# Performance work log

Hardware: AMD Instinct MI355X
Metric: run time of the kernel (lower is better)

The kernel has to match this reference:

```python
import jax, jax.numpy as jnp
import numpy as np

B, N, D, H = 8, 1024, 768, 12
HD = D // H  # head_dim = 64


def setup_inputs() -> dict:
    key = jax.random.key(0)
    k1, k2 = jax.random.split(key)
    x = jax.random.normal(k1, (B, N, D), dtype=jnp.float32)
    W_qkv = jax.random.normal(k2, (D, 3 * D), dtype=jnp.float32) * 0.02
    b_qkv = jnp.zeros((3 * D,), dtype=jnp.float32)
    return {"x": x, "W_qkv": W_qkv, "b_qkv": b_qkv}


def reference(x, W_qkv, b_qkv):
    b, n, d = x.shape
    qkv = x @ W_qkv + b_qkv                      # [B, N, 3D]
    qkv = qkv.reshape(b, n, 3, H, HD)
    qkv = jnp.transpose(qkv, (2, 0, 3, 1, 4))    # [3, B, H, N, HD]
    q, k, v = qkv[0], qkv[1], qkv[2]
    scale = 1.0 / jnp.sqrt(jnp.float32(HD))
    scores = jnp.einsum('bhqd,bhkd->bhqk', q, k) * scale   # [B, H, N, N]
    attn = jax.nn.softmax(scores, axis=-1)
    out = jnp.einsum('bhqk,bhkd->bhqd', attn, v)            # [B, H, N, HD]
    # concat heads along last dim (same as torch.cat over head outputs)
    return jnp.transpose(out, (0, 2, 1, 3)).reshape(b, n, d)
```

## Files before the change

### kernel.cpp

```cpp
#include <hip/hip_runtime.h>
#include <stdint.h>

#define BB 8
#define NN 1024
#define DDIM 768
#define HH 12
#define HDIM 64
#define D3 2304
#define MM 8192

typedef __attribute__((ext_vector_type(4))) float f32x4;
typedef __attribute__((ext_vector_type(16))) float f32x16;
typedef __attribute__((ext_vector_type(8))) __bf16 bf16x8;
typedef __attribute__((ext_vector_type(8))) unsigned short u16x8;
typedef __attribute__((ext_vector_type(4))) unsigned short u16x4;

__device__ __forceinline__ unsigned short f2bf(float f) {
  unsigned int u = __float_as_uint(f);
  u += 0x7FFFu + ((u >> 16) & 1u);
  return (unsigned short)(u >> 16);
}

__device__ __forceinline__ void gload_lds16(const void* g, void* l) {
  __builtin_amdgcn_global_load_lds((const __attribute__((address_space(1))) void*)g,
                                   (__attribute__((address_space(3))) void*)l,
                                   16, 0, 0);
}

__device__ __forceinline__ unsigned cvtpk_bf16(float lo, float hi) {
  unsigned r;
  asm("v_cvt_pk_bf16_f32 %0, %1, %2" : "=v"(r) : "v"(lo), "v"(hi));
  return r;
}

__device__ __forceinline__ bf16x8 mkfrag(unsigned a, unsigned b, unsigned c, unsigned d) {
  union { unsigned u[4]; bf16x8 v; } x;
  x.u[0] = a; x.u[1] = b; x.u[2] = c; x.u[3] = d;
  return x.v;
}

#if __has_builtin(__builtin_amdgcn_exp2f)
#define EXP2(x) __builtin_amdgcn_exp2f(x)
#else
#define EXP2(x) exp2f(x)
#endif

#define QSCL 0.18033688f

__global__ void k_prep(const float4* __restrict__ x, u16x4* __restrict__ xb,
                       const float* __restrict__ W, unsigned short* __restrict__ Wt) {
  __shared__ float tile[32][33];
  const int bid = blockIdx.x;
  if (bid < 6144) {
    int i = bid * 256 + threadIdx.x;
    float4 v = x[i];
    u16x4 o;
    o[0] = f2bf(v.x); o[1] = f2bf(v.y); o[2] = f2bf(v.z); o[3] = f2bf(v.w);
    xb[i] = o;
    return;
  }
  const int bid2 = bid - 6144;
  const int tx = threadIdx.x & 31, ty = threadIdx.x >> 5;
  const int n0 = (bid2 % 72) * 32;
  const int k0 = (bid2 / 72) * 32;
  for (int i = 0; i < 4; ++i) {
    int k = k0 + ty + i * 8;
    tile[ty + i * 8][tx] = W[(size_t)k * D3 + n0 + tx];
  }
  __syncthreads();
  for (int i = 0; i < 4; ++i) {
    int n = n0 + ty + i * 8;
    Wt[(size_t)n * DDIM + k0 + tx] = f2bf(tile[tx][ty + i * 8]);
  }
}

__global__ __launch_bounds__(256, 3)
void k_gemm(const unsigned short* __restrict__ A, const unsigned short* __restrict__ Bt,
            const float* __restrict__ bias, unsigned short* __restrict__ C) {
  __shared__ char lds[48 * 1024];
  const int t = threadIdx.x, lane = t & 63, wid = t >> 6;
  const int orig = blockIdx.x;
  const int xcd = orig & 7, tt = orig >> 3;
  const int m0 = (xcd * 8 + (tt & 7)) * 128;
  const int n0 = (tt >> 3) * 128;
  const int wr = wid >> 1, wc = wid & 1;
  const int grp = lane >> 4, lc = lane & 15;

  f32x4 acc[4][4];
  for (int i = 0; i < 4; ++i)
    for (int j = 0; j < 4; ++j) acc[i][j] = (f32x4)(0.0f);

  auto STAGE = [&](int buf, int kt) {
    char* Ab = lds + buf * 16384;
    char* Bb = Ab + 8192;
#pragma unroll
    for (int i = 0; i < 2; ++i) {
      int chunk = wid * 2 + i;
      int g = chunk * 64 + lane;
      int row = g >> 2, c16 = (g & 3) << 4;
      gload_lds16((const char*)A + (size_t)(m0 + row) * 1536 + kt * 64 + c16, Ab + chunk * 1024);
      gload_lds16((const char*)Bt + (size_t)(n0 + row) * 1536 + kt * 64 + c16, Bb + chunk * 1024);
    }
  };

  STAGE(0, 0);
  asm volatile("s_waitcnt vmcnt(0)" ::: "memory");
  __builtin_amdgcn_s_barrier();

  int cur = 0;
  for (int kt = 0; kt < 24; ++kt) {
    const int nxt = (cur == 2) ? 0 : cur + 1;
    if (kt < 23) {
      STAGE(nxt, kt + 1);
      asm volatile("s_waitcnt vmcnt(4)" ::: "memory");
    } else {
      asm volatile("s_waitcnt vmcnt(0)" ::: "memory");
    }
    __builtin_amdgcn_s_barrier();

    const char* As = lds + cur * 16384;
    const char* Bs = As + 8192;
    bf16x8 af[4], bfr[4];
#pragma unroll
    for (int f = 0; f < 4; ++f) {
      af[f]  = *(const bf16x8*)(As + (wr * 64 + f * 16 + lc) * 64 + grp * 16);
      bfr[f] = *(const bf16x8*)(Bs + (wc * 64 + f * 16 + lc) * 64 + grp * 16);
    }
    __builtin_amdgcn_s_setprio(1);
#pragma unroll
    for (int mf = 0; mf < 4; ++mf)
#pragma unroll
      for (int nf = 0; nf < 4; ++nf)
        acc[mf][nf] = __builtin_amdgcn_mfma_f32_16x16x32_bf16(af[mf], bfr[nf], acc[mf][nf], 0, 0, 0);
    __builtin_amdgcn_s_setprio(0);
    cur = nxt;
  }

  float bv[4];
  float qs[4];
  for (int nf = 0; nf < 4; ++nf) {
    bv[nf] = bias[n0 + wc * 64 + nf * 16 + lc];
    qs[nf] = (n0 + wc * 64 + nf * 16) < DDIM ? QSCL : 1.0f;
  }
  for (int mf = 0; mf < 4; ++mf)
    for (int nf = 0; nf < 4; ++nf)
      for (int i = 0; i < 4; ++i) {
        int r = m0 + wr * 64 + mf * 16 + grp * 4 + i;
        int c = n0 + wc * 64 + nf * 16 + lc;
        C[(size_t)r * D3 + c] = f2bf((acc[mf][nf][i] + bv[nf]) * qs[nf]);
      }
}

__global__ void k_pack(const unsigned short* __restrict__ qkv,
                       unsigned short* __restrict__ kp, unsigned short* __restrict__ vp) {
  __shared__ unsigned short KT[64][68];
  __shared__ unsigned short VT[64][68];
  const int bh = blockIdx.x, kt = blockIdx.y;
  const int b = bh / HH, h = bh % HH;
  const int n0 = kt * 64;
  const int t = threadIdx.x;
#pragma unroll
  for (int it = 0; it < 2; ++it) {
    int id = it * 256 + t;
    int row = id >> 3, seg = id & 7;
    const unsigned short* src = qkv + (size_t)(b * NN + n0 + row) * D3 + DDIM + h * HDIM + seg * 8;
    *(u16x8*)&KT[row][seg * 8] = *(const u16x8*)src;
    *(u16x8*)&VT[row][seg * 8] = *(const u16x8*)(src + DDIM);
  }
  __syncthreads();
  const size_t base = (size_t)(bh * 16 + kt) * 4096;
#pragma unroll
  for (int it = 0; it < 2; ++it) {
    int w = it * 256 + t;
    int c = w >> 6, lane = w & 63;
    int hi2 = lane >> 5, l31 = lane & 31;
    int half = c & 1, quad = c >> 1;
    {
      int row = half * 32 + l31, seg = quad * 2 + hi2;
      *(u16x8*)(kp + base + (size_t)w * 8) = *(const u16x8*)&KT[row][seg * 8];
    }
    {
      int d = half * 32 + l31, nloc = quad * 16 + hi2 * 8;
      u16x8 o;
#pragma unroll
      for (int j = 0; j < 8; ++j) o[j] = VT[nloc + j][d];
      *(u16x8*)(vp + base + (size_t)w * 8) = o;
    }
  }
}

__global__ __launch_bounds__(256, 3)
void k_attn(const unsigned short* __restrict__ qkv,
            const unsigned short* __restrict__ kp, const unsigned short* __restrict__ vp,
            float* __restrict__ out) {
  __shared__ char lds[48 * 1024];
  const int lane = threadIdx.x & 63, wid = threadIdx.x >> 6;
  const int orig = blockIdx.x;
  const int wg = (orig & 7) * 96 + (orig >> 3);
  const int bh = wg >> 3, qt = wg & 7;
  const int b = bh / HH, h = bh % HH;
  const int q0 = qt * 128 + wid * 32;
  const int l31 = lane & 31, hi = lane >> 5;

  auto STAGE = [&](int bi, int kt2) {
    char* buf = lds + bi * 16384;
    const char* gk = (const char*)kp + (size_t)(bh * 16 + kt2) * 8192 + lane * 16;
    const char* gv = (const char*)vp + (size_t)(bh * 16 + kt2) * 8192 + lane * 16;
#pragma unroll
    for (int i = 0; i < 4; ++i) {
      int e = wid * 4 + i;
      const char* g = (e < 8) ? (gk + e * 1024) : (gv + (e - 8) * 1024);
      char* l = (e < 8) ? (buf + e * 1024) : (buf + 8192 + (e - 8) * 1024);
      gload_lds16(g, l);
    }
  };

  STAGE(0, 0);

  bf16x8 qf[4];
  const char* qbase = (const char*)qkv + ((size_t)(b * NN + q0 + l31) * D3 + h * HDIM) * 2;
#pragma unroll
  for (int ds_ = 0; ds_ < 4; ++ds_)
    qf[ds_] = *(const bf16x8*)(qbase + ds_ * 32 + hi * 16);

  f32x16 acc0 = (f32x16)(0.0f), acc1 = (f32x16)(0.0f);
  float l = 0.0f;

  asm volatile("s_waitcnt vmcnt(0)" ::: "memory");
  __builtin_amdgcn_s_barrier();

  int cur = 0;
  for (int kt = 0; kt < 16; ++kt) {
    const int nxt = (cur == 2) ? 0 : cur + 1;
    if (kt < 15) {
      STAGE(nxt, kt + 1);
      asm volatile("s_waitcnt vmcnt(4)" ::: "memory");
    } else {
      asm volatile("s_waitcnt vmcnt(0)" ::: "memory");
    }
    __builtin_amdgcn_s_barrier();

    const char* Kc = lds + cur * 16384;
    const char* Vc = Kc + 8192;

    bf16x8 kf[4][2];
#pragma unroll
    for (int ds_ = 0; ds_ < 4; ++ds_)
#pragma unroll
      for (int r = 0; r < 2; ++r)
        kf[ds_][r] = *(const bf16x8*)(Kc + (ds_ * 2 + r) * 1024 + lane * 16);

    f32x16 st0 = (f32x16)(0.0f), st1 = (f32x16)(0.0f);
    __builtin_amdgcn_s_setprio(1);
#pragma unroll
    for (int ds_ = 0; ds_ < 4; ++ds_) {
      st0 = __builtin_amdgcn_mfma_f32_32x32x16_bf16(kf[ds_][0], qf[ds_], st0, 0, 0, 0);
      st1 = __builtin_amdgcn_mfma_f32_32x32x16_bf16(kf[ds_][1], qf[ds_], st1, 0, 0, 0);
    }
    __builtin_amdgcn_s_setprio(0);

    bf16x8 vf[4][2];
#pragma unroll
    for (int cc = 0; cc < 4; ++cc)
#pragma unroll
      for (int r = 0; r < 2; ++r)
        vf[cc][r] = *(const bf16x8*)(Vc + (cc * 2 + r) * 1024 + lane * 16);

    float s0 = 0.f, s1 = 0.f, s2 = 0.f, s3 = 0.f;
#pragma unroll
    for (int i = 0; i < 16; i += 4) {
      float p0 = EXP2(st0[i]);
      float p1 = EXP2(st0[i + 1]);
      float p2 = EXP2(st0[i + 2]);
      float p3 = EXP2(st0[i + 3]);
      st0[i] = p0; st0[i + 1] = p1; st0[i + 2] = p2; st0[i + 3] = p3;
      s0 += p0; s1 += p1; s2 += p2; s3 += p3;
    }
#pragma unroll
    for (int i = 0; i < 16; i += 4) {
      float p0 = EXP2(st1[i]);
      float p1 = EXP2(st1[i + 1]);
      float p2 = EXP2(st1[i + 2]);
      float p3 = EXP2(st1[i + 3]);
      st1[i] = p0; st1[i + 1] = p1; st1[i + 2] = p2; st1[i + 3] = p3;
      s0 += p0; s1 += p1; s2 += p2; s3 += p3;
    }
    l += (s0 + s1) + (s2 + s3);

#pragma unroll
    for (int kblk = 0; kblk < 2; ++kblk) {
      const f32x16& sp = kblk ? st1 : st0;
      unsigned c0 = cvtpk_bf16(sp[0], sp[1]),   c1 = cvtpk_bf16(sp[2], sp[3]);
      unsigned c2 = cvtpk_bf16(sp[4], sp[5]),   c3 = cvtpk_bf16(sp[6], sp[7]);
      unsigned c4 = cvtpk_bf16(sp[8], sp[9]),   c5 = cvtpk_bf16(sp[10], sp[11]);
      unsigned c6 = cvtpk_bf16(sp[12], sp[13]), c7 = cvtpk_bf16(sp[14], sp[15]);
      unsigned z0 = hi ? c0 : c2, z1 = hi ? c1 : c3;
      unsigned z2 = hi ? c4 : c6, z3 = hi ? c5 : c7;
      unsigned w0 = __shfl_xor(z0, 32, 64), w1 = __shfl_xor(z1, 32, 64);
      unsigned w2 = __shfl_xor(z2, 32, 64), w3 = __shfl_xor(z3, 32, 64);
      bf16x8 pf0 = mkfrag(hi ? w0 : c0, hi ? w1 : c1, hi ? c2 : w0, hi ? c3 : w1);
      bf16x8 pf1 = mkfrag(hi ? w2 : c4, hi ? w3 : c5, hi ? c6 : w2, hi ? c7 : w3);

      __builtin_amdgcn_s_setprio(1);
#pragma unroll
      for (int ch = 0; ch < 2; ++ch) {
        const int cc = kblk * 2 + ch;
        const bf16x8 pf = ch ? pf1 : pf0;
        acc0 = __builtin_amdgcn_mfma_f32_32x32x16_bf16(vf[cc][0], pf, acc0, 0, 0, 0);
        acc1 = __builtin_amdgcn_mfma_f32_32x32x16_bf16(vf[cc][1], pf, acc1, 0, 0, 0);
      }
      __builtin_amdgcn_s_setprio(0);
    }

    cur = nxt;
  }

  float lf = l + __shfl_xor(l, 32, 64);
  float inv = 1.0f / lf;
  float* obase = out + (size_t)(b * NN + q0 + l31) * DDIM + h * HDIM + hi * 4;
#pragma unroll
  for (int rq = 0; rq < 4; ++rq) {
    f32x4 o;
    o[0] = acc0[rq * 4] * inv; o[1] = acc0[rq * 4 + 1] * inv;
    o[2] = acc0[rq * 4 + 2] * inv; o[3] = acc0[rq * 4 + 3] * inv;
    *(f32x4*)(obase + rq * 8) = o;
  }
#pragma unroll
  for (int rq = 0; rq < 4; ++rq) {
    f32x4 o;
    o[0] = acc1[rq * 4] * inv; o[1] = acc1[rq * 4 + 1] * inv;
    o[2] = acc1[rq * 4 + 2] * inv; o[3] = acc1[rq * 4 + 3] * inv;
    *(f32x4*)(obase + 32 + rq * 8) = o;
  }
}

extern "C" void kernel_launch(void* const* d_in, const int* in_sizes, int n_in,
                              void* d_out, int out_size, void* d_ws, size_t ws_size,
                              hipStream_t stream) {
  const float* x = (const float*)d_in[0];
  const float* W = (const float*)d_in[1];
  const float* bqkv = (const float*)d_in[2];
  float* out = (float*)d_out;
  char* ws = (char*)d_ws;

  const size_t XB_OFF = 0;
  const size_t WT_OFF = 12582912;
  const size_t QKV_OFF = WT_OFF + 3538944;
  const size_t VP_OFF = QKV_OFF + 37748736;
  unsigned short* xb = (unsigned short*)(ws + XB_OFF);
  unsigned short* wt = (unsigned short*)(ws + WT_OFF);
  unsigned short* qkvb = (unsigned short*)(ws + QKV_OFF);
  unsigned short* kpk = (unsigned short*)(ws + XB_OFF);
  unsigned short* vpk = (unsigned short*)(ws + VP_OFF);

  k_prep<<<dim3(6144 + 1728), dim3(256), 0, stream>>>((const float4*)x, (u16x4*)xb, W, wt);
  k_gemm<<<dim3(1152), dim3(256), 0, stream>>>(xb, wt, bqkv, qkvb);
  k_pack<<<dim3(BB * HH, NN / 64), dim3(256), 0, stream>>>(qkvb, kpk, vpk);
  k_attn<<<dim3(768), dim3(256), 0, stream>>>(qkvb, kpk, vpk, out);
}
```

Before: 97.63 us.

## Prefetch two stages ahead and store GEMM tiles in fragment-major LDS order

Both the QKV GEMM and the attention kernel now issue global-to-LDS loads two K-tiles ahead across the triple buffer. The next-tile prefetch moves from before the wait to after the MFMA compute, and the prologue vmcnt(0) plus barrier is dropped. This is meant to hide more global-load latency behind compute. The GEMM staging also reorders A/B tiles in LDS so each wave's 16x32 fragment is one contiguous 1 KB chunk read at lane*16. That replaces the previous 64-byte row-strided reads, which likely caused LDS bank conflicts. The cost is more outstanding loads per thread and slightly more complex address math.

```diff
diff --git a/kernel.cpp b/kernel.cpp
--- a/kernel.cpp
+++ b/kernel.cpp
@@ -90,28 +90,29 @@
   for (int i = 0; i < 4; ++i)
     for (int j = 0; j < 4; ++j) acc[i][j] = (f32x4)(0.0f);
 
+  const int srow = lane & 15;
+  const int scol = (lane >> 4) << 4;
+
   auto STAGE = [&](int buf, int kt) {
-    char* Ab = lds + buf * 16384;
-    char* Bb = Ab + 8192;
-#pragma unroll
-    for (int i = 0; i < 2; ++i) {
-      int chunk = wid * 2 + i;
-      int g = chunk * 64 + lane;
-      int row = g >> 2, c16 = (g & 3) << 4;
-      gload_lds16((const char*)A + (size_t)(m0 + row) * 1536 + kt * 64 + c16, Ab + chunk * 1024);
-      gload_lds16((const char*)Bt + (size_t)(n0 + row) * 1536 + kt * 64 + c16, Bb + chunk * 1024);
+    char* base = lds + buf * 16384;
+#pragma unroll
+    for (int i = 0; i < 4; ++i) {
+      int e = wid * 4 + i;
+      int c = e & 7;
+      int row = c * 16 + srow;
+      const char* src = (e < 8)
+        ? (const char*)A  + (size_t)(m0 + row) * 1536 + kt * 64 + scol
+        : (const char*)Bt + (size_t)(n0 + row) * 1536 + kt * 64 + scol;
+      gload_lds16(src, base + e * 1024);
     }
   };
 
   STAGE(0, 0);
-  asm volatile("s_waitcnt vmcnt(0)" ::: "memory");
-  __builtin_amdgcn_s_barrier();
+  STAGE(1, 1);
 
   int cur = 0;
   for (int kt = 0; kt < 24; ++kt) {
-    const int nxt = (cur == 2) ? 0 : cur + 1;
     if (kt < 23) {
-      STAGE(nxt, kt + 1);
       asm volatile("s_waitcnt vmcnt(4)" ::: "memory");
     } else {
       asm volatile("s_waitcnt vmcnt(0)" ::: "memory");
@@ -123,8 +124,8 @@
     bf16x8 af[4], bfr[4];
 #pragma unroll
     for (int f = 0; f < 4; ++f) {
-      af[f]  = *(const bf16x8*)(As + (wr * 64 + f * 16 + lc) * 64 + grp * 16);
-      bfr[f] = *(const bf16x8*)(Bs + (wc * 64 + f * 16 + lc) * 64 + grp * 16);
+      af[f]  = *(const bf16x8*)(As + (wr * 4 + f) * 1024 + lane * 16);
+      bfr[f] = *(const bf16x8*)(Bs + (wc * 4 + f) * 1024 + lane * 16);
     }
     __builtin_amdgcn_s_setprio(1);
 #pragma unroll
@@ -133,7 +134,12 @@
       for (int nf = 0; nf < 4; ++nf)
         acc[mf][nf] = __builtin_amdgcn_mfma_f32_16x16x32_bf16(af[mf], bfr[nf], acc[mf][nf], 0, 0, 0);
     __builtin_amdgcn_s_setprio(0);
-    cur = nxt;
+
+    if (kt + 2 < 24) {
+      int nx = cur + 2; if (nx >= 3) nx -= 3;
+      STAGE(nx, kt + 2);
+    }
+    cur = (cur == 2) ? 0 : cur + 1;
   }
 
   float bv[4];
@@ -215,25 +221,21 @@
     }
   };
 
-  STAGE(0, 0);
-
   bf16x8 qf[4];
   const char* qbase = (const char*)qkv + ((size_t)(b * NN + q0 + l31) * D3 + h * HDIM) * 2;
 #pragma unroll
   for (int ds_ = 0; ds_ < 4; ++ds_)
     qf[ds_] = *(const bf16x8*)(qbase + ds_ * 32 + hi * 16);
 
+  STAGE(0, 0);
+  STAGE(1, 1);
+
   f32x16 acc0 = (f32x16)(0.0f), acc1 = (f32x16)(0.0f);
   float l = 0.0f;
 
-  asm volatile("s_waitcnt vmcnt(0)" ::: "memory");
-  __builtin_amdgcn_s_barrier();
-
   int cur = 0;
   for (int kt = 0; kt < 16; ++kt) {
-    const int nxt = (cur == 2) ? 0 : cur + 1;
     if (kt < 15) {
-      STAGE(nxt, kt + 1);
       asm volatile("s_waitcnt vmcnt(4)" ::: "memory");
     } else {
       asm volatile("s_waitcnt vmcnt(0)" ::: "memory");
@@ -312,7 +314,11 @@
       __builtin_amdgcn_s_setprio(0);
     }
 
-    cur = nxt;
+    if (kt + 2 < 16) {
+      int nx = cur + 2; if (nx >= 3) nx -= 3;
+      STAGE(nx, kt + 2);
+    }
+    cur = (cur == 2) ? 0 : cur + 1;
   }
 
   float lf = l + __shfl_xor(l, 32, 64);
```

Result: slower. 115.0 us (+17.8%).

## Fuse K/V packing into GEMM epilogue and deepen attention prefetch

Applied to the files above, without the earlier changes.

The GEMM epilogue now writes Q into a compact bf16 buffer and writes K and V straight into the packed MFMA-friendly layouts, transposing V through LDS. This removes the separate k_pack launch and the round trip of the full qkv tensor through global memory. The attention kernel also issues its first two tile loads up front and prefetches two tiles ahead within its triple buffer. The cost is LDS staging and extra barriers in the GEMM epilogue, plus more workspace for separate K and V buffers.

```diff
diff --git a/kernel.cpp b/kernel.cpp
--- a/kernel.cpp
+++ b/kernel.cpp
@@ -76,7 +76,8 @@
 
 __global__ __launch_bounds__(256, 3)
 void k_gemm(const unsigned short* __restrict__ A, const unsigned short* __restrict__ Bt,
-            const float* __restrict__ bias, unsigned short* __restrict__ C) {
+            const float* __restrict__ bias, unsigned short* __restrict__ qb,
+            unsigned short* __restrict__ kp, unsigned short* __restrict__ vp) {
   __shared__ char lds[48 * 1024];
   const int t = threadIdx.x, lane = t & 63, wid = t >> 6;
   const int orig = blockIdx.x;
@@ -137,60 +138,64 @@
   }
 
   float bv[4];
-  float qs[4];
-  for (int nf = 0; nf < 4; ++nf) {
-    bv[nf] = bias[n0 + wc * 64 + nf * 16 + lc];
-    qs[nf] = (n0 + wc * 64 + nf * 16) < DDIM ? QSCL : 1.0f;
-  }
-  for (int mf = 0; mf < 4; ++mf)
-    for (int nf = 0; nf < 4; ++nf)
-      for (int i = 0; i < 4; ++i) {
-        int r = m0 + wr * 64 + mf * 16 + grp * 4 + i;
-        int c = n0 + wc * 64 + nf * 16 + lc;
-        C[(size_t)r * D3 + c] = f2bf((acc[mf][nf][i] + bv[nf]) * qs[nf]);
-      }
-}
-
-__global__ void k_pack(const unsigned short* __restrict__ qkv,
-                       unsigned short* __restrict__ kp, unsigned short* __restrict__ vp) {
-  __shared__ unsigned short KT[64][68];
-  __shared__ unsigned short VT[64][68];
-  const int bh = blockIdx.x, kt = blockIdx.y;
-  const int b = bh / HH, h = bh % HH;
-  const int n0 = kt * 64;
-  const int t = threadIdx.x;
-#pragma unroll
-  for (int it = 0; it < 2; ++it) {
-    int id = it * 256 + t;
-    int row = id >> 3, seg = id & 7;
-    const unsigned short* src = qkv + (size_t)(b * NN + n0 + row) * D3 + DDIM + h * HDIM + seg * 8;
-    *(u16x8*)&KT[row][seg * 8] = *(const u16x8*)src;
-    *(u16x8*)&VT[row][seg * 8] = *(const u16x8*)(src + DDIM);
-  }
-  __syncthreads();
-  const size_t base = (size_t)(bh * 16 + kt) * 4096;
-#pragma unroll
-  for (int it = 0; it < 2; ++it) {
-    int w = it * 256 + t;
-    int c = w >> 6, lane = w & 63;
-    int hi2 = lane >> 5, l31 = lane & 31;
-    int half = c & 1, quad = c >> 1;
-    {
-      int row = half * 32 + l31, seg = quad * 2 + hi2;
-      *(u16x8*)(kp + base + (size_t)w * 8) = *(const u16x8*)&KT[row][seg * 8];
-    }
-    {
-      int d = half * 32 + l31, nloc = quad * 16 + hi2 * 8;
-      u16x8 o;
-#pragma unroll
-      for (int j = 0; j < 8; ++j) o[j] = VT[nloc + j][d];
-      *(u16x8*)(vp + base + (size_t)w * 8) = o;
-    }
+#pragma unroll
+  for (int nf = 0; nf < 4; ++nf) bv[nf] = bias[n0 + wc * 64 + nf * 16 + lc];
+
+  const int nt = n0 >> 7;
+  if (nt < 6) {
+#pragma unroll
+    for (int mf = 0; mf < 4; ++mf)
+#pragma unroll
+      for (int nf = 0; nf < 4; ++nf)
+#pragma unroll
+        for (int i = 0; i < 4; ++i) {
+          int r = m0 + wr * 64 + mf * 16 + grp * 4 + i;
+          int c = n0 + wc * 64 + nf * 16 + lc;
+          qb[(size_t)r * DDIM + c] = f2bf((acc[mf][nf][i] + bv[nf]) * QSCL);
+        }
+  } else {
+    __syncthreads();
+    unsigned short* lt = (unsigned short*)lds + wid * 4608;
+    const int l31 = lane & 31, hi2 = lane >> 5;
+    const int bb = m0 >> 10;
+    const int kt_ = ((m0 & 1023) >> 6) + wr;
+    size_t base;
+    unsigned short* dst;
+    if (nt < 12) {
+      const int h = ((n0 - DDIM) >> 6) + wc;
+      base = ((size_t)(bb * HH + h) * 16 + kt_) * 4096;
+      dst = kp;
+#pragma unroll
+      for (int mf = 0; mf < 4; ++mf)
+#pragma unroll
+        for (int nf = 0; nf < 4; ++nf)
+#pragma unroll
+          for (int i = 0; i < 4; ++i)
+            lt[(mf * 16 + grp * 4 + i) * 72 + nf * 16 + lc] = f2bf(acc[mf][nf][i] + bv[nf]);
+    } else {
+      const int h = ((n0 - 2 * DDIM) >> 6) + wc;
+      base = ((size_t)(bb * HH + h) * 16 + kt_) * 4096;
+      dst = vp;
+#pragma unroll
+      for (int mf = 0; mf < 4; ++mf)
+#pragma unroll
+        for (int nf = 0; nf < 4; ++nf)
+#pragma unroll
+          for (int i = 0; i < 4; ++i)
+            lt[(nf * 16 + lc) * 72 + mf * 16 + grp * 4 + i] = f2bf(acc[mf][nf][i] + bv[nf]);
+    }
+    __syncthreads();
+#pragma unroll
+    for (int c2 = 0; c2 < 4; ++c2)
+#pragma unroll
+      for (int r = 0; r < 2; ++r)
+        *(u16x8*)(dst + base + ((size_t)(c2 * 2 + r) * 64 + lane) * 8) =
+          *(const u16x8*)&lt[(r * 32 + l31) * 72 + c2 * 16 + hi2 * 8];
   }
 }
 
 __global__ __launch_bounds__(256, 3)
-void k_attn(const unsigned short* __restrict__ qkv,
+void k_attn(const unsigned short* __restrict__ qb,
             const unsigned short* __restrict__ kp, const unsigned short* __restrict__ vp,
             float* __restrict__ out) {
   __shared__ char lds[48 * 1024];
@@ -215,30 +220,30 @@
     }
   };
 
-  STAGE(0, 0);
-
   bf16x8 qf[4];
-  const char* qbase = (const char*)qkv + ((size_t)(b * NN + q0 + l31) * D3 + h * HDIM) * 2;
+  const char* qbase = (const char*)qb + ((size_t)(b * NN + q0 + l31) * DDIM + h * HDIM) * 2;
 #pragma unroll
   for (int ds_ = 0; ds_ < 4; ++ds_)
     qf[ds_] = *(const bf16x8*)(qbase + ds_ * 32 + hi * 16);
 
+  STAGE(0, 0);
+  STAGE(1, 1);
+
   f32x16 acc0 = (f32x16)(0.0f), acc1 = (f32x16)(0.0f);
   float l = 0.0f;
 
-  asm volatile("s_waitcnt vmcnt(0)" ::: "memory");
-  __builtin_amdgcn_s_barrier();
-
   int cur = 0;
   for (int kt = 0; kt < 16; ++kt) {
-    const int nxt = (cur == 2) ? 0 : cur + 1;
     if (kt < 15) {
-      STAGE(nxt, kt + 1);
       asm volatile("s_waitcnt vmcnt(4)" ::: "memory");
     } else {
       asm volatile("s_waitcnt vmcnt(0)" ::: "memory");
     }
     __builtin_amdgcn_s_barrier();
+    if (kt + 2 < 16) {
+      int nx = cur + 2; if (nx >= 3) nx -= 3;
+      STAGE(nx, kt + 2);
+    }
 
     const char* Kc = lds + cur * 16384;
     const char* Vc = Kc + 8192;
@@ -312,7 +317,7 @@
       __builtin_amdgcn_s_setprio(0);
     }
 
-    cur = nxt;
+    cur = (cur == 2) ? 0 : cur + 1;
   }
 
   float lf = l + __shfl_xor(l, 32, 64);
@@ -345,16 +350,16 @@
 
   const size_t XB_OFF = 0;
   const size_t WT_OFF = 12582912;
-  const size_t QKV_OFF = WT_OFF + 3538944;
-  const size_t VP_OFF = QKV_OFF + 37748736;
+  const size_t QB_OFF = WT_OFF + 3538944;
+  const size_t KP_OFF = QB_OFF + 12582912;
+  const size_t VP_OFF = KP_OFF + 12582912;
   unsigned short* xb = (unsigned short*)(ws + XB_OFF);
   unsigned short* wt = (unsigned short*)(ws + WT_OFF);
-  unsigned short* qkvb = (unsigned short*)(ws + QKV_OFF);
-  unsigned short* kpk = (unsigned short*)(ws + XB_OFF);
+  unsigned short* qbf = (unsigned short*)(ws + QB_OFF);
+  unsigned short* kpk = (unsigned short*)(ws + KP_OFF);
   unsigned short* vpk = (unsigned short*)(ws + VP_OFF);
 
   k_prep<<<dim3(6144 + 1728), dim3(256), 0, stream>>>((const float4*)x, (u16x4*)xb, W, wt);
-  k_gemm<<<dim3(1152), dim3(256), 0, stream>>>(xb, wt, bqkv, qkvb);
-  k_pack<<<dim3(BB * HH, NN / 64), dim3(256), 0, stream>>>(qkvb, kpk, vpk);
-  k_attn<<<dim3(768), dim3(256), 0, stream>>>(qkvb, kpk, vpk, out);
-}
+  k_gemm<<<dim3(1152), dim3(256), 0, stream>>>(xb, wt, bqkv, qbf, kpk, vpk);
+  k_attn<<<dim3(768), dim3(256), 0, stream>>>(qbf, kpk, vpk, out);
+}
```

Measured after the change: 87.76 us. -10.1%, faster.
